# Optimization experiments

Hardware: AMD Instinct MI355X
Metric: run time of the kernel (lower is better)

The kernel has to match this reference:

```python
import jax, jax.numpy as jnp
import numpy as np

VOCAB, EMB, SEQ, BATCH, UNITS = 10000, 100, 80, 1024, 512


def setup_inputs() -> dict:
    key = jax.random.key(0)
    ks = jax.random.split(key, 8)
    s = 0.05  # small init scale to keep gates in a sane range
    return {
        "tokens": jax.random.randint(ks[0], (BATCH, SEQ), 0, VOCAB, dtype=jnp.int64 if jax.config.jax_enable_x64 else jnp.int32),
        "emb": jax.random.normal(ks[1], (VOCAB, EMB), jnp.float32) * s,
        "W1": jax.random.normal(ks[2], (EMB, 4 * UNITS), jnp.float32) * s,
        "U1": jax.random.normal(ks[3], (UNITS, 4 * UNITS), jnp.float32) * s,
        "b1": jnp.zeros((4 * UNITS,), jnp.float32),
        "W2": jax.random.normal(ks[4], (UNITS, 4 * UNITS), jnp.float32) * s,
        "U2": jax.random.normal(ks[5], (UNITS, 4 * UNITS), jnp.float32) * s,
        "b2": jnp.zeros((4 * UNITS,), jnp.float32),
        "Wout": jax.random.normal(ks[6], (UNITS, 1), jnp.float32) * s,
        "bout": jnp.zeros((1,), jnp.float32),
    }


def _lstm_step(x, h, c, W, U, b):
    # Keras LSTMCell gate order: i, f, g(cell), o
    z = x @ W + h @ U + b  # [B, 4*units]
    i, f, g, o = jnp.split(z, 4, axis=-1)
    c_new = jax.nn.sigmoid(f) * c + jax.nn.sigmoid(i) * jnp.tanh(g)
    h_new = jax.nn.sigmoid(o) * jnp.tanh(c_new)
    return h_new, c_new


def reference(tokens, emb, W1, U1, b1, W2, U2, b2, Wout, bout):
    x = emb[tokens]                 # [B, T, E]
    xt = jnp.swapaxes(x, 0, 1)      # [T, B, E] for scan over time
    B = tokens.shape[0]
    units = U1.shape[0]
    zero = jnp.zeros((B, units), x.dtype)

    def step(carry, x_t):
        h1, c1, h2, c2 = carry
        h1, c1 = _lstm_step(x_t, h1, c1, W1, U1, b1)
        h2, c2 = _lstm_step(h1, h2, c2, W2, U2, b2)
        return (h1, c1, h2, c2), None

    (h1, c1, h2, c2), _ = jax.lax.scan(step, (zero, zero, zero, zero), xt)
    return jax.nn.sigmoid(h2 @ Wout + bout)  # [B, 1]
```

## Files before the change

kernel.cpp:

```cpp
#include <hip/hip_runtime.h>
#include <hip/hip_bf16.h>
#include <stdint.h>


#define B_ 1024
#define T_ 80

using bf16 = __hip_bfloat16;
typedef __attribute__((ext_vector_type(8))) short short8;
typedef __attribute__((ext_vector_type(4))) float f32x4;
typedef __attribute__((ext_vector_type(4))) unsigned short ushort4v;

__device__ __forceinline__ float sigf(float x) { return 1.f / (1.f + __expf(-x)); }
__device__ __forceinline__ float tanh_f(float x) { return 2.f / (1.f + __expf(-2.f * x)) - 1.f; }

typedef const __attribute__((address_space(1))) void* gp1_t;
typedef __attribute__((address_space(3))) void* lp3_t;
__device__ __forceinline__ void llds16(const void* g, void* l) {
  __builtin_amdgcn_global_load_lds((gp1_t)g, (lp3_t)l, 16, 0, 0);
}

__global__ void embed_kernel(const int* __restrict__ tokens, const float* __restrict__ emb,
                             bf16* __restrict__ XP) {
  int idx = blockIdx.x * 256 + threadIdx.x;
  int e = idx & 127;
  int bt = idx >> 7;
  int b = bt & (B_ - 1);
  int t = bt >> 10;
  if (t >= T_) return;
  int tok = tokens[b * T_ + t];
  float v = (e < 100) ? emb[tok * 100 + e] : 0.f;
  XP[idx] = __float2bfloat16(v);
}

__global__ void transpose_kernel(const float* __restrict__ W, bf16* __restrict__ WT,
                                 int Kreal, int Kp) {
  __shared__ float tile[32][33];
  int tn = blockIdx.x * 32;
  int tk = blockIdx.y * 32;
  int lx = threadIdx.x & 31;
  int ly = threadIdx.x >> 5;
#pragma unroll
  for (int r = ly; r < 32; r += 8) {
    int k = tk + r;
    tile[r][lx] = (k < Kreal) ? W[(size_t)k * 2048 + tn + lx] : 0.f;
  }
  __syncthreads();
#pragma unroll
  for (int r = ly; r < 32; r += 8) {
    WT[(size_t)(tn + r) * Kp + tk + lx] = __float2bfloat16(tile[lx][r]);
  }
}

struct CellParams {
  const bf16* A0; const bf16* B0;
  const bf16* A1; const bf16* B1;
  int lda0, ldb0, nkt0, lda1, ldb1, nkt1;
  const float* bias; float* C; bf16* H;
};

__global__ __launch_bounds__(512) void cell_kernel(CellParams p0, CellParams p1) {
  __shared__ alignas(16) char smem[65536];
  const CellParams& p = (blockIdx.x >> 7) ? p1 : p0;
  const int lb = blockIdx.x & 127;
  const int g = (lb & 7) | ((lb >> 6) << 3);
  const int bm = (lb >> 3) & 7;
  const int u0 = g * 32;
  const int tid = threadIdx.x;
  const int w = tid >> 6, l = tid & 63, q = l >> 4, m = l & 15;
  const int wm = w >> 2, wn = w & 3;

  const bf16* arow0 = p.A0 + (size_t)(bm * 128 + w * 16 + m) * p.lda0;
  const bf16* brow0 = p.B0 + (size_t)((w >> 1) * 512 + u0 + (w & 1) * 16 + m) * p.ldb0;
  const bf16* arow1 = p.A1 + (size_t)(bm * 128 + w * 16 + m) * p.lda1;
  const bf16* brow1 = p.B1 + (size_t)((w >> 1) * 512 + u0 + (w & 1) * 16 + m) * p.ldb1;

  auto stage = [&](int kt, int buf) {
    const bf16 *ga, *gb;
    if (kt < p.nkt0) { int k0 = kt * 32 + q * 8; ga = arow0 + k0; gb = brow0 + k0; }
    else { int k0 = (kt - p.nkt0) * 32 + q * 8; ga = arow1 + k0; gb = brow1 + k0; }
    char* base = smem + buf * 16384 + w * 1024;
    llds16(ga, base);
    llds16(gb, base + 8192);
  };

  f32x4 acc[4][2];
#pragma unroll
  for (int mi = 0; mi < 4; ++mi)
#pragma unroll
    for (int nj = 0; nj < 2; ++nj) acc[mi][nj] = (f32x4){0.f, 0.f, 0.f, 0.f};

  const int fbase = q * 256 + m * 16;
  const int total = p.nkt0 + p.nkt1;
  stage(0, 0);
  stage(1, 1);
  stage(2, 2);
  for (int kt = 0; kt < total; ++kt) {
    const int rem = total - 1 - kt;
    if (rem >= 2)      asm volatile("s_waitcnt vmcnt(4)" ::: "memory");
    else if (rem == 1) asm volatile("s_waitcnt vmcnt(2)" ::: "memory");
    else               asm volatile("s_waitcnt vmcnt(0)" ::: "memory");
    __builtin_amdgcn_s_barrier();
    if (kt + 3 < total) stage(kt + 3, (kt + 3) & 3);
    const int cb = (kt & 3) * 16384;
    short8 a[4], b[2];
#pragma unroll
    for (int mi = 0; mi < 4; ++mi)
      a[mi] = *(const short8*)(smem + cb + (wm * 4 + mi) * 1024 + fbase);
#pragma unroll
    for (int nj = 0; nj < 2; ++nj)
      b[nj] = *(const short8*)(smem + cb + 8192 + (wn * 2 + nj) * 1024 + fbase);
#pragma unroll
    for (int mi = 0; mi < 4; ++mi)
#pragma unroll
      for (int nj = 0; nj < 2; ++nj)
        acc[mi][nj] = __builtin_amdgcn_mfma_f32_16x16x32_bf16(a[mi], b[nj], acc[mi][nj], 0, 0, 0);
  }

  __syncthreads();
  float* zs = (float*)smem;
  const int erow = tid >> 3;
  const int ub = (tid & 7) * 4;
  float bi[4], bff[4], bg[4], bo[4];
#pragma unroll
  for (int j = 0; j < 4; ++j) {
    int gu = u0 + ub + j;
    bi[j] = p.bias[gu];
    bff[j] = p.bias[512 + gu];
    bg[j] = p.bias[1024 + gu];
    bo[j] = p.bias[1536 + gu];
  }
#pragma unroll
  for (int pass = 0; pass < 2; ++pass) {
    if (pass) __syncthreads();
    if (wm == pass) {
#pragma unroll
      for (int mi = 0; mi < 4; ++mi)
#pragma unroll
        for (int nj = 0; nj < 2; ++nj)
#pragma unroll
          for (int r = 0; r < 4; ++r)
            zs[(mi * 16 + q * 4 + r) * 133 + wn * 32 + nj * 16 + m] = acc[mi][nj][r];
    }
    __syncthreads();
    int grow = bm * 128 + pass * 64 + erow;
    size_t gi = (size_t)grow * 512 + u0 + ub;
    float4 cold = *(const float4*)(p.C + gi);
    float cn[4];
    unsigned short hv[4];
#pragma unroll
    for (int j = 0; j < 4; ++j) {
      float zi = zs[erow * 133 + ub + j] + bi[j];
      float zf = zs[erow * 133 + 32 + ub + j] + bff[j];
      float zg = zs[erow * 133 + 64 + ub + j] + bg[j];
      float zo = zs[erow * 133 + 96 + ub + j] + bo[j];
      float co = (j == 0) ? cold.x : (j == 1) ? cold.y : (j == 2) ? cold.z : cold.w;
      float c = sigf(zf) * co + sigf(zi) * tanh_f(zg);
      float h = sigf(zo) * tanh_f(c);
      cn[j] = c;
      bf16 hb = __float2bfloat16(h);
      hv[j] = *(unsigned short*)&hb;
    }
    *(float4*)(p.C + gi) = make_float4(cn[0], cn[1], cn[2], cn[3]);
    *(ushort4v*)(p.H + gi) = (ushort4v){hv[0], hv[1], hv[2], hv[3]};
  }
}

__global__ void output_kernel(const bf16* __restrict__ H2, const float* __restrict__ Wout,
                              const float* __restrict__ bout, float* __restrict__ out) {
  int w = threadIdx.x >> 6, l = threadIdx.x & 63;
  int row = blockIdx.x * 4 + w;
  const bf16* h = H2 + (size_t)row * 512;
  float s = 0.f;
#pragma unroll
  for (int k = 0; k < 8; ++k) {
    int kk = l + k * 64;
    s += __bfloat162float(h[kk]) * Wout[kk];
  }
#pragma unroll
  for (int off = 32; off > 0; off >>= 1) s += __shfl_down(s, off);
  if (l == 0) out[row] = sigf(s + bout[0]);
}

extern "C" void kernel_launch(void* const* d_in, const int* in_sizes, int n_in,
                              void* d_out, int out_size, void* d_ws, size_t ws_size,
                              hipStream_t stream) {
  const int* tokens = (const int*)d_in[0];
  const float* emb = (const float*)d_in[1];
  const float* W1 = (const float*)d_in[2];
  const float* U1 = (const float*)d_in[3];
  const float* b1 = (const float*)d_in[4];
  const float* W2 = (const float*)d_in[5];
  const float* U2 = (const float*)d_in[6];
  const float* b2 = (const float*)d_in[7];
  const float* Wout = (const float*)d_in[8];
  const float* bout = (const float*)d_in[9];
  float* out = (float*)d_out;
  char* ws = (char*)d_ws;

  const size_t oXP = 0;
  const size_t oW1T = 20971520;
  const size_t oU1T = 21495808;
  const size_t oW2T = 23592960;
  const size_t oU2T = 25690112;
  const size_t oH1 = 27787264;
  const size_t oH2 = 29884416;
  const size_t oC1 = 31981568;
  const size_t oC2 = 34078720;
  if (ws_size < 36175872) return;

  bf16* XP = (bf16*)(ws + oXP);
  bf16* W1T = (bf16*)(ws + oW1T);
  bf16* U1T = (bf16*)(ws + oU1T);
  bf16* W2T = (bf16*)(ws + oW2T);
  bf16* U2T = (bf16*)(ws + oU2T);
  bf16* H1 = (bf16*)(ws + oH1);
  bf16* H2 = (bf16*)(ws + oH2);
  float* C1 = (float*)(ws + oC1);
  float* C2 = (float*)(ws + oC2);

  hipMemsetAsync(ws + oH1, 0, 1048576, stream);
  hipMemsetAsync(ws + oH2, 0, 1048576, stream);
  hipMemsetAsync(ws + oC1, 0, 4194304, stream);

  embed_kernel<<<40960, 256, 0, stream>>>(tokens, emb, XP);
  transpose_kernel<<<dim3(64, 4), 256, 0, stream>>>(W1, W1T, 100, 128);
  transpose_kernel<<<dim3(64, 16), 256, 0, stream>>>(U1, U1T, 512, 512);
  transpose_kernel<<<dim3(64, 16), 256, 0, stream>>>(W2, W2T, 512, 512);
  transpose_kernel<<<dim3(64, 16), 256, 0, stream>>>(U2, U2T, 512, 512);

  auto mkL1 = [&](int t) {
    CellParams p;
    p.A0 = XP + (size_t)t * 131072; p.B0 = W1T; p.lda0 = 128; p.ldb0 = 128; p.nkt0 = 4;
    p.A1 = H1 + (size_t)(t & 1) * 524288; p.B1 = U1T; p.lda1 = 512; p.ldb1 = 512; p.nkt1 = 16;
    p.bias = b1; p.C = C1; p.H = H1 + (size_t)((t + 1) & 1) * 524288;
    return p;
  };
  auto mkL2 = [&](int t) {
    CellParams p;
    p.A0 = H1 + (size_t)((t + 1) & 1) * 524288; p.B0 = W2T; p.lda0 = 512; p.ldb0 = 512; p.nkt0 = 16;
    p.A1 = H2 + (size_t)(t & 1) * 524288; p.B1 = U2T; p.lda1 = 512; p.ldb1 = 512; p.nkt1 = 16;
    p.bias = b2; p.C = C2; p.H = H2 + (size_t)((t + 1) & 1) * 524288;
    return p;
  };

  cell_kernel<<<128, 512, 0, stream>>>(mkL1(0), mkL1(0));
  for (int k = 1; k < T_; ++k)
    cell_kernel<<<256, 512, 0, stream>>>(mkL2(k - 1), mkL1(k));
  cell_kernel<<<128, 512, 0, stream>>>(mkL2(T_ - 1), mkL2(T_ - 1));

  output_kernel<<<256, 256, 0, stream>>>(H2, Wout, bout, out);
}
```

Before: 1.778 ms.

## Double K-tile depth in LSTM cell GEMM, single-pass epilogue, vectorize embedding

The cell kernel now stages 64-wide K tiles instead of 32-wide tiles. It uses a 4-stage 128KB LDS ring and issues two MFMA groups per barrier, which halves the number of barrier and waitcnt iterations per step. The gate epilogue writes all 128 rows to LDS at once and processes 8 units per thread with vectorized bias, C and H accesses, replacing the earlier two-pass scheme. The embedding gather is also vectorized to 8 elements per thread. The larger LDS footprint limits occupancy to one block per CU, and the deeper prefetch raises the outstanding-load count.

```diff
diff --git a/kernel.cpp b/kernel.cpp
--- a/kernel.cpp
+++ b/kernel.cpp
@@ -9,7 +9,7 @@
 using bf16 = __hip_bfloat16;
 typedef __attribute__((ext_vector_type(8))) short short8;
 typedef __attribute__((ext_vector_type(4))) float f32x4;
-typedef __attribute__((ext_vector_type(4))) unsigned short ushort4v;
+typedef __attribute__((ext_vector_type(8))) unsigned short ushort8v;
 
 __device__ __forceinline__ float sigf(float x) { return 1.f / (1.f + __expf(-x)); }
 __device__ __forceinline__ float tanh_f(float x) { return 2.f / (1.f + __expf(-2.f * x)) - 1.f; }
@@ -23,14 +23,31 @@
 __global__ void embed_kernel(const int* __restrict__ tokens, const float* __restrict__ emb,
                              bf16* __restrict__ XP) {
   int idx = blockIdx.x * 256 + threadIdx.x;
-  int e = idx & 127;
-  int bt = idx >> 7;
+  int j = idx & 15;
+  int bt = idx >> 4;
   int b = bt & (B_ - 1);
   int t = bt >> 10;
   if (t >= T_) return;
   int tok = tokens[b * T_ + t];
-  float v = (e < 100) ? emb[tok * 100 + e] : 0.f;
-  XP[idx] = __float2bfloat16(v);
+  int e0 = j * 8;
+  float v[8];
+  if (e0 + 8 <= 100) {
+    *(float4*)(v) = *(const float4*)(emb + (size_t)tok * 100 + e0);
+    *(float4*)(v + 4) = *(const float4*)(emb + (size_t)tok * 100 + e0 + 4);
+  } else if (e0 < 100) {
+    *(float4*)(v) = *(const float4*)(emb + (size_t)tok * 100 + e0);
+    v[4] = v[5] = v[6] = v[7] = 0.f;
+  } else {
+#pragma unroll
+    for (int k = 0; k < 8; ++k) v[k] = 0.f;
+  }
+  ushort8v o;
+#pragma unroll
+  for (int k = 0; k < 8; ++k) {
+    bf16 hb = __float2bfloat16(v[k]);
+    o[k] = *(unsigned short*)&hb;
+  }
+  *(ushort8v*)(XP + (size_t)bt * 128 + e0) = o;
 }
 
 __global__ void transpose_kernel(const float* __restrict__ W, bf16* __restrict__ WT,
@@ -59,8 +76,8 @@
   const float* bias; float* C; bf16* H;
 };
 
-__global__ __launch_bounds__(512) void cell_kernel(CellParams p0, CellParams p1) {
-  __shared__ alignas(16) char smem[65536];
+__global__ __launch_bounds__(512, 1) void cell_kernel(CellParams p0, CellParams p1) {
+  __shared__ alignas(16) char smem[131072];
   const CellParams& p = (blockIdx.x >> 7) ? p1 : p0;
   const int lb = blockIdx.x & 127;
   const int g = (lb & 7) | ((lb >> 6) << 3);
@@ -77,11 +94,13 @@
 
   auto stage = [&](int kt, int buf) {
     const bf16 *ga, *gb;
-    if (kt < p.nkt0) { int k0 = kt * 32 + q * 8; ga = arow0 + k0; gb = brow0 + k0; }
-    else { int k0 = (kt - p.nkt0) * 32 + q * 8; ga = arow1 + k0; gb = brow1 + k0; }
-    char* base = smem + buf * 16384 + w * 1024;
-    llds16(ga, base);
-    llds16(gb, base + 8192);
+    if (kt < p.nkt0) { int k0 = kt * 64 + q * 8; ga = arow0 + k0; gb = brow0 + k0; }
+    else { int k0 = (kt - p.nkt0) * 64 + q * 8; ga = arow1 + k0; gb = brow1 + k0; }
+    char* ab = smem + buf * 32768 + w * 2048;
+    llds16(ga, ab);
+    llds16(ga + 32, ab + 1024);
+    llds16(gb, ab + 16384);
+    llds16(gb + 32, ab + 16384 + 1024);
   };
 
   f32x4 acc[4][2];
@@ -92,78 +111,100 @@
 
   const int fbase = q * 256 + m * 16;
   const int total = p.nkt0 + p.nkt1;
+
   stage(0, 0);
   stage(1, 1);
   stage(2, 2);
   for (int kt = 0; kt < total; ++kt) {
     const int rem = total - 1 - kt;
-    if (rem >= 2)      asm volatile("s_waitcnt vmcnt(4)" ::: "memory");
-    else if (rem == 1) asm volatile("s_waitcnt vmcnt(2)" ::: "memory");
+    if (rem >= 2)      asm volatile("s_waitcnt vmcnt(8)" ::: "memory");
+    else if (rem == 1) asm volatile("s_waitcnt vmcnt(4)" ::: "memory");
     else               asm volatile("s_waitcnt vmcnt(0)" ::: "memory");
     __builtin_amdgcn_s_barrier();
+    __builtin_amdgcn_sched_barrier(0);
     if (kt + 3 < total) stage(kt + 3, (kt + 3) & 3);
-    const int cb = (kt & 3) * 16384;
-    short8 a[4], b[2];
-#pragma unroll
-    for (int mi = 0; mi < 4; ++mi)
-      a[mi] = *(const short8*)(smem + cb + (wm * 4 + mi) * 1024 + fbase);
+    const int cb = (kt & 3) * 32768;
+    short8 a0[4], b0[2], a1[4], b1[2];
+#pragma unroll
+    for (int mi = 0; mi < 4; ++mi)
+      a0[mi] = *(const short8*)(smem + cb + (wm * 4 + mi) * 2048 + fbase);
 #pragma unroll
     for (int nj = 0; nj < 2; ++nj)
-      b[nj] = *(const short8*)(smem + cb + 8192 + (wn * 2 + nj) * 1024 + fbase);
+      b0[nj] = *(const short8*)(smem + cb + 16384 + (wn * 2 + nj) * 2048 + fbase);
+#pragma unroll
+    for (int mi = 0; mi < 4; ++mi)
+      a1[mi] = *(const short8*)(smem + cb + (wm * 4 + mi) * 2048 + 1024 + fbase);
+#pragma unroll
+    for (int nj = 0; nj < 2; ++nj)
+      b1[nj] = *(const short8*)(smem + cb + 16384 + (wn * 2 + nj) * 2048 + 1024 + fbase);
 #pragma unroll
     for (int mi = 0; mi < 4; ++mi)
 #pragma unroll
       for (int nj = 0; nj < 2; ++nj)
-        acc[mi][nj] = __builtin_amdgcn_mfma_f32_16x16x32_bf16(a[mi], b[nj], acc[mi][nj], 0, 0, 0);
+        acc[mi][nj] = __builtin_amdgcn_mfma_f32_16x16x32_bf16(a0[mi], b0[nj], acc[mi][nj], 0, 0, 0);
+#pragma unroll
+    for (int mi = 0; mi < 4; ++mi)
+#pragma unroll
+      for (int nj = 0; nj < 2; ++nj)
+        acc[mi][nj] = __builtin_amdgcn_mfma_f32_16x16x32_bf16(a1[mi], b1[nj], acc[mi][nj], 0, 0, 0);
   }
 
   __syncthreads();
   float* zs = (float*)smem;
-  const int erow = tid >> 3;
-  const int ub = (tid & 7) * 4;
-  float bi[4], bff[4], bg[4], bo[4];
-#pragma unroll
-  for (int j = 0; j < 4; ++j) {
-    int gu = u0 + ub + j;
-    bi[j] = p.bias[gu];
-    bff[j] = p.bias[512 + gu];
-    bg[j] = p.bias[1024 + gu];
-    bo[j] = p.bias[1536 + gu];
-  }
-#pragma unroll
-  for (int pass = 0; pass < 2; ++pass) {
-    if (pass) __syncthreads();
-    if (wm == pass) {
-#pragma unroll
-      for (int mi = 0; mi < 4; ++mi)
-#pragma unroll
-        for (int nj = 0; nj < 2; ++nj)
-#pragma unroll
-          for (int r = 0; r < 4; ++r)
-            zs[(mi * 16 + q * 4 + r) * 133 + wn * 32 + nj * 16 + m] = acc[mi][nj][r];
-    }
-    __syncthreads();
-    int grow = bm * 128 + pass * 64 + erow;
-    size_t gi = (size_t)grow * 512 + u0 + ub;
-    float4 cold = *(const float4*)(p.C + gi);
-    float cn[4];
-    unsigned short hv[4];
-#pragma unroll
-    for (int j = 0; j < 4; ++j) {
-      float zi = zs[erow * 133 + ub + j] + bi[j];
-      float zf = zs[erow * 133 + 32 + ub + j] + bff[j];
-      float zg = zs[erow * 133 + 64 + ub + j] + bg[j];
-      float zo = zs[erow * 133 + 96 + ub + j] + bo[j];
-      float co = (j == 0) ? cold.x : (j == 1) ? cold.y : (j == 2) ? cold.z : cold.w;
-      float c = sigf(zf) * co + sigf(zi) * tanh_f(zg);
-      float h = sigf(zo) * tanh_f(c);
-      cn[j] = c;
-      bf16 hb = __float2bfloat16(h);
-      hv[j] = *(unsigned short*)&hb;
-    }
-    *(float4*)(p.C + gi) = make_float4(cn[0], cn[1], cn[2], cn[3]);
-    *(ushort4v*)(p.H + gi) = (ushort4v){hv[0], hv[1], hv[2], hv[3]};
-  }
+#pragma unroll
+  for (int mi = 0; mi < 4; ++mi)
+#pragma unroll
+    for (int nj = 0; nj < 2; ++nj)
+#pragma unroll
+      for (int r = 0; r < 4; ++r)
+        zs[(wm * 64 + mi * 16 + q * 4 + r) * 132 + wn * 32 + nj * 16 + m] = acc[mi][nj][r];
+  __syncthreads();
+
+  const int erow = tid >> 2;
+  const int ub8 = (tid & 3) * 8;
+  const int gu0 = u0 + ub8;
+  float bi[8], bfv[8], bg[8], bo[8];
+  *(float4*)(bi) = *(const float4*)(p.bias + gu0);
+  *(float4*)(bi + 4) = *(const float4*)(p.bias + gu0 + 4);
+  *(float4*)(bfv) = *(const float4*)(p.bias + 512 + gu0);
+  *(float4*)(bfv + 4) = *(const float4*)(p.bias + 512 + gu0 + 4);
+  *(float4*)(bg) = *(const float4*)(p.bias + 1024 + gu0);
+  *(float4*)(bg + 4) = *(const float4*)(p.bias + 1024 + gu0 + 4);
+  *(float4*)(bo) = *(const float4*)(p.bias + 1536 + gu0);
+  *(float4*)(bo + 4) = *(const float4*)(p.bias + 1536 + gu0 + 4);
+
+  float zr[32];
+  const float* zrow = zs + erow * 132;
+  *(float4*)(zr) = *(const float4*)(zrow + ub8);
+  *(float4*)(zr + 4) = *(const float4*)(zrow + ub8 + 4);
+  *(float4*)(zr + 8) = *(const float4*)(zrow + 32 + ub8);
+  *(float4*)(zr + 12) = *(const float4*)(zrow + 32 + ub8 + 4);
+  *(float4*)(zr + 16) = *(const float4*)(zrow + 64 + ub8);
+  *(float4*)(zr + 20) = *(const float4*)(zrow + 64 + ub8 + 4);
+  *(float4*)(zr + 24) = *(const float4*)(zrow + 96 + ub8);
+  *(float4*)(zr + 28) = *(const float4*)(zrow + 96 + ub8 + 4);
+
+  const int grow = bm * 128 + erow;
+  const size_t gi = (size_t)grow * 512 + gu0;
+  float cold[8], cn[8];
+  *(float4*)(cold) = *(const float4*)(p.C + gi);
+  *(float4*)(cold + 4) = *(const float4*)(p.C + gi + 4);
+  unsigned short hv[8];
+#pragma unroll
+  for (int j = 0; j < 8; ++j) {
+    float zi = zr[j] + bi[j];
+    float zf = zr[8 + j] + bfv[j];
+    float zg = zr[16 + j] + bg[j];
+    float zo = zr[24 + j] + bo[j];
+    float c = sigf(zf) * cold[j] + sigf(zi) * tanh_f(zg);
+    float h = sigf(zo) * tanh_f(c);
+    cn[j] = c;
+    bf16 hb = __float2bfloat16(h);
+    hv[j] = *(unsigned short*)&hb;
+  }
+  *(float4*)(p.C + gi) = make_float4(cn[0], cn[1], cn[2], cn[3]);
+  *(float4*)(p.C + gi + 4) = make_float4(cn[4], cn[5], cn[6], cn[7]);
+  *(ushort8v*)(p.H + gi) = (ushort8v){hv[0], hv[1], hv[2], hv[3], hv[4], hv[5], hv[6], hv[7]};
 }
 
 __global__ void output_kernel(const bf16* __restrict__ H2, const float* __restrict__ Wout,
@@ -223,7 +264,7 @@
   hipMemsetAsync(ws + oH2, 0, 1048576, stream);
   hipMemsetAsync(ws + oC1, 0, 4194304, stream);
 
-  embed_kernel<<<40960, 256, 0, stream>>>(tokens, emb, XP);
+  embed_kernel<<<5120, 256, 0, stream>>>(tokens, emb, XP);
   transpose_kernel<<<dim3(64, 4), 256, 0, stream>>>(W1, W1T, 100, 128);
   transpose_kernel<<<dim3(64, 16), 256, 0, stream>>>(U1, U1T, 512, 512);
   transpose_kernel<<<dim3(64, 16), 256, 0, stream>>>(W2, W2T, 512, 512);
@@ -231,15 +272,15 @@
 
   auto mkL1 = [&](int t) {
     CellParams p;
-    p.A0 = XP + (size_t)t * 131072; p.B0 = W1T; p.lda0 = 128; p.ldb0 = 128; p.nkt0 = 4;
-    p.A1 = H1 + (size_t)(t & 1) * 524288; p.B1 = U1T; p.lda1 = 512; p.ldb1 = 512; p.nkt1 = 16;
+    p.A0 = XP + (size_t)t * 131072; p.B0 = W1T; p.lda0 = 128; p.ldb0 = 128; p.nkt0 = 2;
+    p.A1 = H1 + (size_t)(t & 1) * 524288; p.B1 = U1T; p.lda1 = 512; p.ldb1 = 512; p.nkt1 = 8;
     p.bias = b1; p.C = C1; p.H = H1 + (size_t)((t + 1) & 1) * 524288;
     return p;
   };
   auto mkL2 = [&](int t) {
     CellParams p;
-    p.A0 = H1 + (size_t)((t + 1) & 1) * 524288; p.B0 = W2T; p.lda0 = 512; p.ldb0 = 512; p.nkt0 = 16;
-    p.A1 = H2 + (size_t)(t & 1) * 524288; p.B1 = U2T; p.lda1 = 512; p.ldb1 = 512; p.nkt1 = 16;
+    p.A0 = H1 + (size_t)((t + 1) & 1) * 524288; p.B0 = W2T; p.lda0 = 512; p.ldb0 = 512; p.nkt0 = 8;
+    p.A1 = H2 + (size_t)(t & 1) * 524288; p.B1 = U2T; p.lda1 = 512; p.ldb1 = 512; p.nkt1 = 8;
     p.bias = b2; p.C = C2; p.H = H2 + (size_t)((t + 1) & 1) * 524288;
     return p;
   };
```

After: 1.765 ms. No clear change (-0.7%).
